# Kernel optimization log

Hardware: AMD Instinct MI355X
Metric: run time of the kernel (lower is better)

## Reference

```python
import jax, jax.numpy as jnp
import numpy as np

N = 50000
E = 800000
IN_C, HID_C, OUT_C = 5, 64, 32


def setup_inputs() -> dict:
    key = jax.random.key(0)
    ks = jax.random.split(key, 9)
    x = jax.random.normal(ks[0], (N, IN_C), dtype=jnp.float32)
    edge_index = jax.random.randint(ks[1], (2, E), 0, N, dtype=jnp.int64)
    # SAGEConv params: lin_l (neighbor path, has bias), lin_r (root path, no bias)
    def lin(k, fan_out, fan_in):
        s = 1.0 / np.sqrt(fan_in)
        return jax.random.uniform(k, (fan_out, fan_in), jnp.float32, -s, s)
    W1l = lin(ks[2], HID_C, IN_C); b1 = jnp.zeros((HID_C,), jnp.float32); W1r = lin(ks[3], HID_C, IN_C)
    W2l = lin(ks[4], HID_C, HID_C); b2 = jnp.zeros((HID_C,), jnp.float32); W2r = lin(ks[5], HID_C, HID_C)
    W3l = lin(ks[6], OUT_C, HID_C); b3 = jnp.zeros((OUT_C,), jnp.float32); W3r = lin(ks[7], OUT_C, HID_C)
    return {"x": x, "edge_index": edge_index,
            "W1l": W1l, "b1": b1, "W1r": W1r,
            "W2l": W2l, "b2": b2, "W2r": W2r,
            "W3l": W3l, "b3": b3, "W3r": W3r}


def _sage_conv(x, src, dst, inv_deg, Wl, bl, Wr):
    # PyG SAGEConv (aggr='mean'): out = lin_l(mean_j x_j) + lin_r(x)
    msg = x[src]                                          # [E, d_in] gather
    agg = jax.ops.segment_sum(msg, dst, num_segments=N)   # [N, d_in] scatter-add
    mean = agg * inv_deg                                  # mean aggregation
    return mean @ Wl.T + bl + x @ Wr.T


def reference(x, edge_index, W1l, b1, W1r, W2l, b2, W2r, W3l, b3, W3r):
    src, dst = edge_index[0], edge_index[1]
    deg = jax.ops.segment_sum(jnp.ones((E,), x.dtype), dst, num_segments=N)
    inv_deg = (1.0 / jnp.maximum(deg, 1.0))[:, None]      # [N, 1]
    h = jax.nn.relu(_sage_conv(x, src, dst, inv_deg, W1l, b1, W1r))
    # F.dropout(p=0.2, training=self.training): identity in eval mode
    h = jax.nn.relu(_sage_conv(h, src, dst, inv_deg, W2l, b2, W2r))
    out = _sage_conv(h, src, dst, inv_deg, W3l, b3, W3r)
    return out
```

## Files before the change

### kernel.cpp

```cpp
#include <hip/hip_runtime.h>
#include <hip/hip_fp16.h>


#define N_NODES 50000
#define N_EDGES 800000
#define IN_C 5
#define HID_C 64
#define OUT_C 32

#define NB 196
#define BCAP 6144
#define BWG 256
#define BCH (N_EDGES / BWG)

typedef __attribute__((ext_vector_type(8))) short bf16x8;
typedef __attribute__((ext_vector_type(4))) float f32x4;

__device__ __forceinline__ int rfl(int v) { return __builtin_amdgcn_readfirstlane(v); }
__device__ __forceinline__ float lanebc(float v, int l) {
    return __int_as_float(__builtin_amdgcn_readlane(__float_as_int(v), l));
}
__device__ __forceinline__ unsigned short f2bf(float f) {
    unsigned u = __float_as_uint(f);
    return (unsigned short)((u + 0x7fffu + ((u >> 16) & 1u)) >> 16);
}
__device__ __forceinline__ float bf2f(unsigned short b) {
    return __uint_as_float(((unsigned)b) << 16);
}
__device__ __forceinline__ float2 unpk_h2(unsigned u) {
    __half2 h = *(__half2*)&u;
    return __half22float2(h);
}


__global__ __launch_bounds__(256) void k_prep(
    const float* __restrict__ W2l, const float* __restrict__ W2r,
    const float* __restrict__ W3l, const float* __restrict__ W3r,
    unsigned short* __restrict__ W2hi, unsigned short* __restrict__ W2lo,
    unsigned short* __restrict__ W3hi, unsigned short* __restrict__ W3lo,
    int* __restrict__ gcur) {
    if (blockIdx.x == 0 && threadIdx.x < NB) gcur[threadIdx.x] = 0;
    const int t = blockIdx.x * 256 + threadIdx.x;
    const int stride = gridDim.x * 256;
    for (int p = t; p < 64 * 128; p += stride) {
        int j = p >> 7, k = p & 127;
        float w = (k < 64) ? W2l[j * 64 + k] : W2r[j * 64 + (k - 64)];
        unsigned short h = f2bf(w);
        W2hi[p] = h;
        W2lo[p] = f2bf(w - bf2f(h));
    }
    for (int p = t; p < 32 * 128; p += stride) {
        int j = p >> 7, k = p & 127;
        float w = (k < 64) ? W3l[j * 64 + k] : W3r[j * 64 + (k - 64)];
        unsigned short h = f2bf(w);
        W3hi[p] = h;
        W3lo[p] = f2bf(w - bf2f(h));
    }
}


__global__ __launch_bounds__(256) void k_bucket(const int* __restrict__ ei,
                                                int* __restrict__ gcur,
                                                unsigned* __restrict__ ebuf) {
    __shared__ int hist[NB];
    __shared__ int loff[NB];
    __shared__ int cur[NB];
    __shared__ int gbase[NB];
    __shared__ int scanb[256];
    __shared__ unsigned stage[BCH];
    const int t = threadIdx.x;
    const int c0 = blockIdx.x * BCH;

    if (t < NB) hist[t] = 0;
    __syncthreads();
    for (int i = t; i < BCH; i += 256) {
        int d = ei[N_EDGES + c0 + i];
        atomicAdd(&hist[d >> 8], 1);
    }
    __syncthreads();
    scanb[t] = (t < NB) ? hist[t] : 0;
    __syncthreads();
#pragma unroll
    for (int o = 1; o < 256; o <<= 1) {
        int v = scanb[t];
        int a = (t >= o) ? scanb[t - o] : 0;
        __syncthreads();
        scanb[t] = v + a;
        __syncthreads();
    }
    if (t < NB) {
        int ex = (t == 0) ? 0 : scanb[t - 1];
        loff[t] = ex;
        cur[t] = ex;
        gbase[t] = atomicAdd(&gcur[t], hist[t]);
    }
    __syncthreads();
    for (int i = t; i < BCH; i += 256) {
        int d = ei[N_EDGES + c0 + i];
        int s = ei[c0 + i];
        int b = d >> 8;
        int p = atomicAdd(&cur[b], 1);
        stage[p] = ((unsigned)d << 16) | (unsigned)s;
    }
    __syncthreads();
    for (int i = t; i < BCH; i += 256) {
        unsigned ev = stage[i];
        int b = ev >> 24;
        int pos = gbase[b] + (i - loff[b]);
        if (pos < BCAP) ebuf[b * BCAP + pos] = ev;
    }
}

__global__ __launch_bounds__(256) void k_bsort(const int* __restrict__ gcur,
                                               const unsigned* __restrict__ ebuf,
                                               int* __restrict__ row_off,
                                               float* __restrict__ inv_deg,
                                               int* __restrict__ srcs) {
    __shared__ int sc[256];
    __shared__ int cnt[256];
    __shared__ int loff[256];
    __shared__ int cur[256];
    __shared__ int stage[BCAP];
    const int t = threadIdx.x;
    const int b = blockIdx.x;

    sc[t] = (t < NB) ? gcur[t] : 0;
    __syncthreads();
#pragma unroll
    for (int o = 1; o < 256; o <<= 1) {
        int v = sc[t];
        int a = (t >= o) ? sc[t - o] : 0;
        __syncthreads();
        sc[t] = v + a;
        __syncthreads();
    }
    const int base = (b == 0) ? 0 : sc[b - 1];
    const int nraw = gcur[b];
    const int n = nraw < BCAP ? nraw : BCAP;
    const int node0 = b << 8;
    const unsigned* eb = ebuf + b * BCAP;

    cnt[t] = 0;
    __syncthreads();
    for (int i = t; i < n; i += 256) atomicAdd(&cnt[(eb[i] >> 16) & 255], 1);
    __syncthreads();
    loff[t] = cnt[t];
    __syncthreads();
#pragma unroll
    for (int o = 1; o < 256; o <<= 1) {
        int v = loff[t];
        int a = (t >= o) ? loff[t - o] : 0;
        __syncthreads();
        loff[t] = v + a;
        __syncthreads();
    }
    int ex = loff[t] - cnt[t];
    cur[t] = ex;
    int node = node0 + t;
    if (node < N_NODES) {
        row_off[node] = base + ex;
        int d = cnt[t];
        inv_deg[node] = 1.0f / (float)(d > 1 ? d : 1);
    }
    if (b == 0 && t == 0) row_off[N_NODES] = N_EDGES;
    __syncthreads();
    for (int i = t; i < n; i += 256) {
        unsigned ev = eb[i];
        int p = atomicAdd(&cur[(ev >> 16) & 255], 1);
        stage[p] = (int)(ev & 0xFFFFu);
    }
    __syncthreads();
    for (int i = t; i < n; i += 256) srcs[base + i] = stage[i];
}


__global__ __launch_bounds__(256) void k_layer1(
    const float* __restrict__ x, const int* __restrict__ row_off,
    const int* __restrict__ srcs, const float* __restrict__ inv_deg,
    const float* __restrict__ W1l, const float* __restrict__ b1,
    const float* __restrict__ W1r, __half* __restrict__ h1) {
    const int t = threadIdx.x;
    const int lane = t & 63;
    const int v = blockIdx.x * 4 + (t >> 6);
    if (v >= N_NODES) return;
    const int sub = lane >> 3;
    const int c = lane & 7;

    float wl[IN_C], wr[IN_C];
#pragma unroll
    for (int i = 0; i < IN_C; ++i) {
        wl[i] = W1l[lane * IN_C + i];
        wr[i] = W1r[lane * IN_C + i];
    }
    float bb = b1[lane];

    int beg = rfl(row_off[v]);
    int end = rfl(row_off[v + 1]);
    float sum = 0.f;
    for (int e = beg; e < end; e += 8) {
        int o = e + sub;
        if (o < end && c < IN_C) sum += x[srcs[o] * IN_C + c];
    }
    sum += __shfl_xor(sum, 8, 64);
    sum += __shfl_xor(sum, 16, 64);
    sum += __shfl_xor(sum, 32, 64);
    float summ = sum * inv_deg[v];
    float xv = (lane < IN_C) ? x[v * IN_C + lane] : 0.f;
    float acc = bb;
#pragma unroll
    for (int i = 0; i < IN_C; ++i) {
        acc += wl[i] * lanebc(summ, i);
        acc += wr[i] * lanebc(xv, i);
    }
    h1[v * HID_C + lane] = __float2half(fmaxf(acc, 0.f));
}


template <typename T> __device__ __forceinline__ T cvt_out(float v);
template <> __device__ __forceinline__ float cvt_out<float>(float v) { return v; }
template <> __device__ __forceinline__ __half cvt_out<__half>(float v) { return __float2half(v); }

template <int DOUT, bool RELU, typename OutT>
__global__ __launch_bounds__(256) void k_fused(
    const __half* __restrict__ h, const int* __restrict__ row_off,
    const int* __restrict__ srcs, const float* __restrict__ inv_deg,
    const unsigned short* __restrict__ Whi, const unsigned short* __restrict__ Wlo,
    const float* __restrict__ bias, OutT* __restrict__ out) {
    constexpr int AP = 152;
    __shared__ __align__(16) unsigned short Ah[32][AP];
    __shared__ __align__(16) unsigned short Al[32][AP];
    const int t = threadIdx.x;
    const int lane = t & 63;
    const int w = t >> 6;
    const int ns = lane >> 3;
    const int cg = lane & 7;
    const int node0 = blockIdx.x * 32;
    const int m = w * 8 + ns;
    const int v = node0 + m;
    const bool valid = v < N_NODES;
    const uint4* h4 = (const uint4*)h;

    int beg = 0, deg = 0;
    if (valid) {
        beg = row_off[v];
        deg = row_off[v + 1] - beg;
    }

    float s0 = 0.f, s1 = 0.f, s2 = 0.f, s3 = 0.f;
    float s4 = 0.f, s5 = 0.f, s6 = 0.f, s7 = 0.f;
    for (int k = 0; k < deg; k += 4) {
        int i0 = srcs[beg + k];
        int i1 = (k + 1 < deg) ? srcs[beg + k + 1] : i0;
        int i2 = (k + 2 < deg) ? srcs[beg + k + 2] : i0;
        int i3 = (k + 3 < deg) ? srcs[beg + k + 3] : i0;
        uint4 u0 = h4[i0 * 8 + cg];
        uint4 u1 = h4[i1 * 8 + cg];
        uint4 u2 = h4[i2 * 8 + cg];
        uint4 u3 = h4[i3 * 8 + cg];
        {
            float2 a = unpk_h2(u0.x), b = unpk_h2(u0.y);
            float2 c = unpk_h2(u0.z), d = unpk_h2(u0.w);
            s0 += a.x; s1 += a.y; s2 += b.x; s3 += b.y;
            s4 += c.x; s5 += c.y; s6 += d.x; s7 += d.y;
        }
        if (k + 1 < deg) {
            float2 a = unpk_h2(u1.x), b = unpk_h2(u1.y);
            float2 c = unpk_h2(u1.z), d = unpk_h2(u1.w);
            s0 += a.x; s1 += a.y; s2 += b.x; s3 += b.y;
            s4 += c.x; s5 += c.y; s6 += d.x; s7 += d.y;
        }
        if (k + 2 < deg) {
            float2 a = unpk_h2(u2.x), b = unpk_h2(u2.y);
            float2 c = unpk_h2(u2.z), d = unpk_h2(u2.w);
            s0 += a.x; s1 += a.y; s2 += b.x; s3 += b.y;
            s4 += c.x; s5 += c.y; s6 += d.x; s7 += d.y;
        }
        if (k + 3 < deg) {
            float2 a = unpk_h2(u3.x), b = unpk_h2(u3.y);
            float2 c = unpk_h2(u3.z), d = unpk_h2(u3.w);
            s0 += a.x; s1 += a.y; s2 += b.x; s3 += b.y;
            s4 += c.x; s5 += c.y; s6 += d.x; s7 += d.y;
        }
    }

    uint4 ur = make_uint4(0u, 0u, 0u, 0u);
    float idg = 0.f;
    if (valid) {
        ur = h4[v * 8 + cg];
        idg = inv_deg[v];
    }
    float m0 = s0 * idg, m1 = s1 * idg, m2 = s2 * idg, m3 = s3 * idg;
    float m4 = s4 * idg, m5 = s5 * idg, m6 = s6 * idg, m7 = s7 * idg;

    {
        unsigned short a0 = f2bf(m0), a1 = f2bf(m1), a2 = f2bf(m2), a3 = f2bf(m3);
        unsigned short a4 = f2bf(m4), a5 = f2bf(m5), a6 = f2bf(m6), a7 = f2bf(m7);
        uint4 hi, lo;
        hi.x = (unsigned)a0 | ((unsigned)a1 << 16);
        hi.y = (unsigned)a2 | ((unsigned)a3 << 16);
        hi.z = (unsigned)a4 | ((unsigned)a5 << 16);
        hi.w = (unsigned)a6 | ((unsigned)a7 << 16);
        lo.x = (unsigned)f2bf(m0 - bf2f(a0)) | ((unsigned)f2bf(m1 - bf2f(a1)) << 16);
        lo.y = (unsigned)f2bf(m2 - bf2f(a2)) | ((unsigned)f2bf(m3 - bf2f(a3)) << 16);
        lo.z = (unsigned)f2bf(m4 - bf2f(a4)) | ((unsigned)f2bf(m5 - bf2f(a5)) << 16);
        lo.w = (unsigned)f2bf(m6 - bf2f(a6)) | ((unsigned)f2bf(m7 - bf2f(a7)) << 16);
        *(uint4*)&Ah[m][cg * 8] = hi;
        *(uint4*)&Al[m][cg * 8] = lo;
    }
    {
        float2 p0 = unpk_h2(ur.x), p1 = unpk_h2(ur.y);
        float2 p2 = unpk_h2(ur.z), p3 = unpk_h2(ur.w);
        unsigned short a0 = f2bf(p0.x), a1 = f2bf(p0.y), a2 = f2bf(p1.x), a3 = f2bf(p1.y);
        unsigned short a4 = f2bf(p2.x), a5 = f2bf(p2.y), a6 = f2bf(p3.x), a7 = f2bf(p3.y);
        uint4 hi, lo;
        hi.x = (unsigned)a0 | ((unsigned)a1 << 16);
        hi.y = (unsigned)a2 | ((unsigned)a3 << 16);
        hi.z = (unsigned)a4 | ((unsigned)a5 << 16);
        hi.w = (unsigned)a6 | ((unsigned)a7 << 16);
        lo.x = (unsigned)f2bf(p0.x - bf2f(a0)) | ((unsigned)f2bf(p0.y - bf2f(a1)) << 16);
        lo.y = (unsigned)f2bf(p1.x - bf2f(a2)) | ((unsigned)f2bf(p1.y - bf2f(a3)) << 16);
        lo.z = (unsigned)f2bf(p2.x - bf2f(a4)) | ((unsigned)f2bf(p2.y - bf2f(a5)) << 16);
        lo.w = (unsigned)f2bf(p3.x - bf2f(a6)) | ((unsigned)f2bf(p3.y - bf2f(a7)) << 16);
        *(uint4*)&Ah[m][64 + cg * 8] = hi;
        *(uint4*)&Al[m][64 + cg * 8] = lo;
    }
    __syncthreads();

    constexpr int CT = DOUT / 16;
    constexpr int NTILES = 2 * CT;
    const int r = lane & 15;
    const int quad = lane >> 4;
#pragma unroll
    for (int ti = w; ti < NTILES; ti += 4) {
        const int n = ti % CT;
        const int rh = ti / CT;
        f32x4 acc = (f32x4){0.f, 0.f, 0.f, 0.f};
#pragma unroll
        for (int ks = 0; ks < 4; ++ks) {
            bf16x8 ah = *(const bf16x8*)&Ah[rh * 16 + r][ks * 32 + quad * 8];
            bf16x8 al = *(const bf16x8*)&Al[rh * 16 + r][ks * 32 + quad * 8];
            const size_t wb = ((size_t)(n * 16 + r)) * 128 + ks * 32 + quad * 8;
            bf16x8 bh = *(const bf16x8*)(Whi + wb);
            bf16x8 bl = *(const bf16x8*)(Wlo + wb);
            acc = __builtin_amdgcn_mfma_f32_16x16x32_bf16(ah, bh, acc, 0, 0, 0);
            acc = __builtin_amdgcn_mfma_f32_16x16x32_bf16(ah, bl, acc, 0, 0, 0);
            acc = __builtin_amdgcn_mfma_f32_16x16x32_bf16(al, bh, acc, 0, 0, 0);
        }
        float bv = bias[n * 16 + r];
#pragma unroll
        for (int g = 0; g < 4; ++g) {
            int node = node0 + rh * 16 + quad * 4 + g;
            if (node < N_NODES) {
                float vv = acc[g] + bv;
                if (RELU) vv = fmaxf(vv, 0.f);
                out[(size_t)node * DOUT + n * 16 + r] = cvt_out<OutT>(vv);
            }
        }
    }
}


extern "C" void kernel_launch(void* const* d_in, const int* in_sizes, int n_in,
                              void* d_out, int out_size, void* d_ws, size_t ws_size,
                              hipStream_t stream) {
    const float* x   = (const float*)d_in[0];
    const int*   ei  = (const int*)d_in[1];
    const float* W1l = (const float*)d_in[2];
    const float* b1  = (const float*)d_in[3];
    const float* W1r = (const float*)d_in[4];
    const float* W2l = (const float*)d_in[5];
    const float* b2  = (const float*)d_in[6];
    const float* W2r = (const float*)d_in[7];
    const float* W3l = (const float*)d_in[8];
    const float* b3  = (const float*)d_in[9];
    const float* W3r = (const float*)d_in[10];

    char* ws = (char*)d_ws;
    size_t off = 0;
    auto alloc = [&](size_t bytes) -> char* {
        char* p = ws + off;
        off += (bytes + 255) & ~(size_t)255;
        return p;
    };
    int*      gcur   = (int*)alloc(NB * sizeof(int));
    int*      rowoff = (int*)alloc((N_NODES + 1) * sizeof(int));
    float*    invdeg = (float*)alloc(N_NODES * sizeof(float));
    int*      srcs   = (int*)alloc(N_EDGES * sizeof(int));
    unsigned* ebuf   = (unsigned*)alloc((size_t)NB * BCAP * sizeof(unsigned));
    __half*   h1     = (__half*)alloc((size_t)N_NODES * HID_C * sizeof(__half));
    __half*   h2     = (__half*)alloc((size_t)N_NODES * HID_C * sizeof(__half));
    unsigned short* W2hi = (unsigned short*)alloc(64 * 128 * 2);
    unsigned short* W2lo = (unsigned short*)alloc(64 * 128 * 2);
    unsigned short* W3hi = (unsigned short*)alloc(32 * 128 * 2);
    unsigned short* W3lo = (unsigned short*)alloc(32 * 128 * 2);

    k_prep<<<dim3(48), dim3(256), 0, stream>>>(W2l, W2r, W3l, W3r,
                                               W2hi, W2lo, W3hi, W3lo, gcur);
    k_bucket<<<dim3(BWG), dim3(256), 0, stream>>>(ei, gcur, ebuf);
    k_bsort<<<dim3(NB), dim3(256), 0, stream>>>(gcur, ebuf, rowoff, invdeg, srcs);

    k_layer1<<<dim3(N_NODES / 4), dim3(256), 0, stream>>>(
        x, rowoff, srcs, invdeg, W1l, b1, W1r, h1);

    const int FT = (N_NODES + 31) / 32;
    k_fused<HID_C, true, __half><<<dim3(FT), dim3(256), 0, stream>>>(
        h1, rowoff, srcs, invdeg, W2hi, W2lo, b2, h2);

    k_fused<OUT_C, false, float><<<dim3(FT), dim3(256), 0, stream>>>(
        h2, rowoff, srcs, invdeg, W3hi, W3lo, b3, (float*)d_out);
}
```

Before: 172.9 us.

## Pad x to fp16 rows, remap layer1 to 8 lanes per node, unroll gather by 8

The prep kernel now converts x into a padded fp16 array of 8 halves per node, so a single 16-byte load fetches a whole row. Layer 1 is remapped so each node uses 8 lanes, with 32 nodes per block instead of 4. Those lanes split the neighbour list, reduce with shuffles, and each computes 8 outputs written as one vector store. The layer 2/3 gather loop is unrolled from 4 to 8 neighbours, giving more loads in flight; the root-row and inv_deg loads are hoisted ahead of it. The cost is an extra prep pass over x, fp16 rounding of the layer-1 inputs, and more registers per thread for weights and the unrolled gather.

New measurement: 177.1 us. 2.4% more time.

```diff
diff --git a/kernel.cpp b/kernel.cpp
--- a/kernel.cpp
+++ b/kernel.cpp
@@ -17,9 +17,6 @@
 typedef __attribute__((ext_vector_type(4))) float f32x4;
 
 __device__ __forceinline__ int rfl(int v) { return __builtin_amdgcn_readfirstlane(v); }
-__device__ __forceinline__ float lanebc(float v, int l) {
-    return __int_as_float(__builtin_amdgcn_readlane(__float_as_int(v), l));
-}
 __device__ __forceinline__ unsigned short f2bf(float f) {
     unsigned u = __float_as_uint(f);
     return (unsigned short)((u + 0x7fffu + ((u >> 16) & 1u)) >> 16);
@@ -34,11 +31,12 @@
 
 
 __global__ __launch_bounds__(256) void k_prep(
+    const float* __restrict__ x,
     const float* __restrict__ W2l, const float* __restrict__ W2r,
     const float* __restrict__ W3l, const float* __restrict__ W3r,
     unsigned short* __restrict__ W2hi, unsigned short* __restrict__ W2lo,
     unsigned short* __restrict__ W3hi, unsigned short* __restrict__ W3lo,
-    int* __restrict__ gcur) {
+    __half* __restrict__ xp, int* __restrict__ gcur) {
     if (blockIdx.x == 0 && threadIdx.x < NB) gcur[threadIdx.x] = 0;
     const int t = blockIdx.x * 256 + threadIdx.x;
     const int stride = gridDim.x * 256;
@@ -55,6 +53,10 @@
         unsigned short h = f2bf(w);
         W3hi[p] = h;
         W3lo[p] = f2bf(w - bf2f(h));
+    }
+    for (int p = t; p < N_NODES * 8; p += stride) {
+        int v = p >> 3, i = p & 7;
+        xp[p] = __float2half((i < IN_C) ? x[v * IN_C + i] : 0.f);
     }
 }
 
@@ -175,44 +177,83 @@
 
 
 __global__ __launch_bounds__(256) void k_layer1(
-    const float* __restrict__ x, const int* __restrict__ row_off,
+    const __half* __restrict__ xp, const int* __restrict__ row_off,
     const int* __restrict__ srcs, const float* __restrict__ inv_deg,
     const float* __restrict__ W1l, const float* __restrict__ b1,
     const float* __restrict__ W1r, __half* __restrict__ h1) {
     const int t = threadIdx.x;
     const int lane = t & 63;
-    const int v = blockIdx.x * 4 + (t >> 6);
-    if (v >= N_NODES) return;
-    const int sub = lane >> 3;
-    const int c = lane & 7;
-
-    float wl[IN_C], wr[IN_C];
-#pragma unroll
-    for (int i = 0; i < IN_C; ++i) {
-        wl[i] = W1l[lane * IN_C + i];
-        wr[i] = W1r[lane * IN_C + i];
-    }
-    float bb = b1[lane];
-
-    int beg = rfl(row_off[v]);
-    int end = rfl(row_off[v + 1]);
-    float sum = 0.f;
-    for (int e = beg; e < end; e += 8) {
-        int o = e + sub;
-        if (o < end && c < IN_C) sum += x[srcs[o] * IN_C + c];
-    }
-    sum += __shfl_xor(sum, 8, 64);
-    sum += __shfl_xor(sum, 16, 64);
-    sum += __shfl_xor(sum, 32, 64);
-    float summ = sum * inv_deg[v];
-    float xv = (lane < IN_C) ? x[v * IN_C + lane] : 0.f;
-    float acc = bb;
-#pragma unroll
-    for (int i = 0; i < IN_C; ++i) {
-        acc += wl[i] * lanebc(summ, i);
-        acc += wr[i] * lanebc(xv, i);
-    }
-    h1[v * HID_C + lane] = __float2half(fmaxf(acc, 0.f));
+    const int ns = lane >> 3;
+    const int j = lane & 7;
+    const int v = blockIdx.x * 32 + (t >> 6) * 8 + ns;
+    const bool valid = v < N_NODES;
+    const uint4* x4 = (const uint4*)xp;
+
+    float wl[8][IN_C], wr[8][IN_C], bb[8];
+#pragma unroll
+    for (int q = 0; q < 8; ++q) {
+        int o = j * 8 + q;
+#pragma unroll
+        for (int i = 0; i < IN_C; ++i) {
+            wl[q][i] = W1l[o * IN_C + i];
+            wr[q][i] = W1r[o * IN_C + i];
+        }
+        bb[q] = b1[o];
+    }
+
+    int beg = 0, deg = 0;
+    float idg = 0.f;
+    if (valid) {
+        beg = row_off[v];
+        deg = row_off[v + 1] - beg;
+        idg = inv_deg[v];
+    }
+    uint4 ur = valid ? x4[v] : make_uint4(0u, 0u, 0u, 0u);
+
+    float a0 = 0.f, a1 = 0.f, a2 = 0.f, a3 = 0.f, a4 = 0.f;
+    for (int k = j; k < deg; k += 16) {
+        int i0 = srcs[beg + k];
+        int k1 = k + 8;
+        int i1 = (k1 < deg) ? srcs[beg + k1] : i0;
+        uint4 u0 = x4[i0];
+        uint4 u1 = x4[i1];
+        float2 p0 = unpk_h2(u0.x), p1 = unpk_h2(u0.y), p2 = unpk_h2(u0.z);
+        a0 += p0.x; a1 += p0.y; a2 += p1.x; a3 += p1.y; a4 += p2.x;
+        if (k1 < deg) {
+            float2 q0 = unpk_h2(u1.x), q1 = unpk_h2(u1.y), q2 = unpk_h2(u1.z);
+            a0 += q0.x; a1 += q0.y; a2 += q1.x; a3 += q1.y; a4 += q2.x;
+        }
+    }
+#pragma unroll
+    for (int msk = 1; msk < 8; msk <<= 1) {
+        a0 += __shfl_xor(a0, msk, 64);
+        a1 += __shfl_xor(a1, msk, 64);
+        a2 += __shfl_xor(a2, msk, 64);
+        a3 += __shfl_xor(a3, msk, 64);
+        a4 += __shfl_xor(a4, msk, 64);
+    }
+    float mean[IN_C] = {a0 * idg, a1 * idg, a2 * idg, a3 * idg, a4 * idg};
+    float2 r0 = unpk_h2(ur.x), r1 = unpk_h2(ur.y), r2 = unpk_h2(ur.z);
+    float root[IN_C] = {r0.x, r0.y, r1.x, r1.y, r2.x};
+
+    unsigned short res[8];
+#pragma unroll
+    for (int q = 0; q < 8; ++q) {
+        float acc = bb[q];
+#pragma unroll
+        for (int i = 0; i < IN_C; ++i)
+            acc += wl[q][i] * mean[i] + wr[q][i] * root[i];
+        acc = fmaxf(acc, 0.f);
+        res[q] = __half_as_ushort(__float2half(acc));
+    }
+    if (valid) {
+        uint4 o;
+        o.x = (unsigned)res[0] | ((unsigned)res[1] << 16);
+        o.y = (unsigned)res[2] | ((unsigned)res[3] << 16);
+        o.z = (unsigned)res[4] | ((unsigned)res[5] << 16);
+        o.w = (unsigned)res[6] | ((unsigned)res[7] << 16);
+        ((uint4*)(h1 + (size_t)v * HID_C))[j] = o;
+    }
 }
 
 
@@ -241,54 +282,71 @@
     const uint4* h4 = (const uint4*)h;
 
     int beg = 0, deg = 0;
+    float idg = 0.f;
+    uint4 ur = make_uint4(0u, 0u, 0u, 0u);
     if (valid) {
         beg = row_off[v];
         deg = row_off[v + 1] - beg;
+        idg = inv_deg[v];
+        ur = h4[v * 8 + cg];
     }
 
     float s0 = 0.f, s1 = 0.f, s2 = 0.f, s3 = 0.f;
     float s4 = 0.f, s5 = 0.f, s6 = 0.f, s7 = 0.f;
-    for (int k = 0; k < deg; k += 4) {
+#define ACC8(U) do {                                                \
+        float2 _a = unpk_h2((U).x), _b = unpk_h2((U).y);            \
+        float2 _c = unpk_h2((U).z), _d = unpk_h2((U).w);            \
+        s0 += _a.x; s1 += _a.y; s2 += _b.x; s3 += _b.y;             \
+        s4 += _c.x; s5 += _c.y; s6 += _d.x; s7 += _d.y;             \
+    } while (0)
+
+    const int kfull = deg & ~7;
+    int k = 0;
+    for (; k < kfull; k += 8) {
+        int i0 = srcs[beg + k + 0];
+        int i1 = srcs[beg + k + 1];
+        int i2 = srcs[beg + k + 2];
+        int i3 = srcs[beg + k + 3];
+        int i4 = srcs[beg + k + 4];
+        int i5 = srcs[beg + k + 5];
+        int i6 = srcs[beg + k + 6];
+        int i7 = srcs[beg + k + 7];
+        uint4 u0 = h4[i0 * 8 + cg];
+        uint4 u1 = h4[i1 * 8 + cg];
+        uint4 u2 = h4[i2 * 8 + cg];
+        uint4 u3 = h4[i3 * 8 + cg];
+        uint4 u4 = h4[i4 * 8 + cg];
+        uint4 u5 = h4[i5 * 8 + cg];
+        uint4 u6 = h4[i6 * 8 + cg];
+        uint4 u7 = h4[i7 * 8 + cg];
+        ACC8(u0); ACC8(u1); ACC8(u2); ACC8(u3);
+        ACC8(u4); ACC8(u5); ACC8(u6); ACC8(u7);
+    }
+    if (k < deg) {
         int i0 = srcs[beg + k];
         int i1 = (k + 1 < deg) ? srcs[beg + k + 1] : i0;
         int i2 = (k + 2 < deg) ? srcs[beg + k + 2] : i0;
         int i3 = (k + 3 < deg) ? srcs[beg + k + 3] : i0;
+        int i4 = (k + 4 < deg) ? srcs[beg + k + 4] : i0;
+        int i5 = (k + 5 < deg) ? srcs[beg + k + 5] : i0;
+        int i6 = (k + 6 < deg) ? srcs[beg + k + 6] : i0;
         uint4 u0 = h4[i0 * 8 + cg];
         uint4 u1 = h4[i1 * 8 + cg];
         uint4 u2 = h4[i2 * 8 + cg];
         uint4 u3 = h4[i3 * 8 + cg];
-        {
-            float2 a = unpk_h2(u0.x), b = unpk_h2(u0.y);
-            float2 c = unpk_h2(u0.z), d = unpk_h2(u0.w);
-            s0 += a.x; s1 += a.y; s2 += b.x; s3 += b.y;
-            s4 += c.x; s5 += c.y; s6 += d.x; s7 += d.y;
-        }
-        if (k + 1 < deg) {
-            float2 a = unpk_h2(u1.x), b = unpk_h2(u1.y);
-            float2 c = unpk_h2(u1.z), d = unpk_h2(u1.w);
-            s0 += a.x; s1 += a.y; s2 += b.x; s3 += b.y;
-            s4 += c.x; s5 += c.y; s6 += d.x; s7 += d.y;
-        }
-        if (k + 2 < deg) {
-            float2 a = unpk_h2(u2.x), b = unpk_h2(u2.y);
-            float2 c = unpk_h2(u2.z), d = unpk_h2(u2.w);
-            s0 += a.x; s1 += a.y; s2 += b.x; s3 += b.y;
-            s4 += c.x; s5 += c.y; s6 += d.x; s7 += d.y;
-        }
-        if (k + 3 < deg) {
-            float2 a = unpk_h2(u3.x), b = unpk_h2(u3.y);
-            float2 c = unpk_h2(u3.z), d = unpk_h2(u3.w);
-            s0 += a.x; s1 += a.y; s2 += b.x; s3 += b.y;
-            s4 += c.x; s5 += c.y; s6 += d.x; s7 += d.y;
-        }
-    }
-
-    uint4 ur = make_uint4(0u, 0u, 0u, 0u);
-    float idg = 0.f;
-    if (valid) {
-        ur = h4[v * 8 + cg];
-        idg = inv_deg[v];
-    }
+        uint4 u4 = h4[i4 * 8 + cg];
+        uint4 u5 = h4[i5 * 8 + cg];
+        uint4 u6 = h4[i6 * 8 + cg];
+        ACC8(u0);
+        if (k + 1 < deg) ACC8(u1);
+        if (k + 2 < deg) ACC8(u2);
+        if (k + 3 < deg) ACC8(u3);
+        if (k + 4 < deg) ACC8(u4);
+        if (k + 5 < deg) ACC8(u5);
+        if (k + 6 < deg) ACC8(u6);
+    }
+#undef ACC8
+
     float m0 = s0 * idg, m1 = s1 * idg, m2 = s2 * idg, m3 = s3 * idg;
     float m4 = s4 * idg, m5 = s5 * idg, m6 = s6 * idg, m7 = s7 * idg;
 
@@ -387,6 +445,7 @@
     float*    invdeg = (float*)alloc(N_NODES * sizeof(float));
     int*      srcs   = (int*)alloc(N_EDGES * sizeof(int));
     unsigned* ebuf   = (unsigned*)alloc((size_t)NB * BCAP * sizeof(unsigned));
+    __half*   xp     = (__half*)alloc((size_t)N_NODES * 8 * sizeof(__half));
     __half*   h1     = (__half*)alloc((size_t)N_NODES * HID_C * sizeof(__half));
     __half*   h2     = (__half*)alloc((size_t)N_NODES * HID_C * sizeof(__half));
     unsigned short* W2hi = (unsigned short*)alloc(64 * 128 * 2);
@@ -394,13 +453,14 @@
     unsigned short* W3hi = (unsigned short*)alloc(32 * 128 * 2);
     unsigned short* W3lo = (unsigned short*)alloc(32 * 128 * 2);
 
-    k_prep<<<dim3(48), dim3(256), 0, stream>>>(W2l, W2r, W3l, W3r,
-                                               W2hi, W2lo, W3hi, W3lo, gcur);
+    k_prep<<<dim3(64), dim3(256), 0, stream>>>(x, W2l, W2r, W3l, W3r,
+                                               W2hi, W2lo, W3hi, W3lo, xp, gcur);
     k_bucket<<<dim3(BWG), dim3(256), 0, stream>>>(ei, gcur, ebuf);
     k_bsort<<<dim3(NB), dim3(256), 0, stream>>>(gcur, ebuf, rowoff, invdeg, srcs);
 
-    k_layer1<<<dim3(N_NODES / 4), dim3(256), 0, stream>>>(
-        x, rowoff, srcs, invdeg, W1l, b1, W1r, h1);
+    const int L1B = (N_NODES + 31) / 32;
+    k_layer1<<<dim3(L1B), dim3(256), 0, stream>>>(
+        xp, rowoff, srcs, invdeg, W1l, b1, W1r, h1);
 
     const int FT = (N_NODES + 31) / 32;
     k_fused<HID_C, true, __half><<<dim3(FT), dim3(256), 0, stream>>>(
```
